# Performance work log

Hardware: AMD Instinct MI355X
Metric: run time of the kernel (lower is better)

Reference implementation:

```python
import jax, jax.numpy as jnp
import numpy as np

N, E, G = 20000, 50000, 64          # nodes, edges, graphs
IN_DIM, EDGE_DIM, H, OUT_DIM = 32, 16, 64, 6
EPS = 1e-5  # BatchNorm eps


def setup_inputs() -> dict:
    key = jax.random.key(0)
    ks = jax.random.split(key, 24)
    s = 0.05
    inp = {
        "x": jax.random.normal(ks[0], (N, IN_DIM), jnp.float32),
        "edge_attr": jax.random.normal(ks[1], (E, EDGE_DIM), jnp.float32),
        "src": jax.random.randint(ks[2], (E,), 0, N, jnp.int32),
        "dst": jax.random.randint(ks[3], (E,), 0, N, jnp.int32),
        "batch": jnp.sort(jax.random.randint(ks[4], (N,), 0, G, jnp.int32)),
        # node encoder
        "Wx": jax.random.normal(ks[5], (IN_DIM, H), jnp.float32) * s,
        "bx": jnp.zeros((H,), jnp.float32),
        # three edge MLPs: edge_dim -> H*H
        "We": jax.random.normal(ks[6], (3, EDGE_DIM, H * H), jnp.float32) * s,
        "be": jnp.zeros((3, H * H), jnp.float32),
        # NNConv root weights / biases
        "Wroot": jax.random.normal(ks[7], (3, H, H), jnp.float32) * s,
        "broot": jnp.zeros((3, H), jnp.float32),
        # BatchNorm (eval mode: running stats)
        "gamma": jnp.ones((3, H), jnp.float32),
        "beta": jnp.zeros((3, H), jnp.float32),
        "run_mean": jnp.zeros((3, H), jnp.float32),
        "run_var": jnp.ones((3, H), jnp.float32),
        # head
        "W1": jax.random.normal(ks[8], (H, H), jnp.float32) * s,
        "b1": jnp.zeros((H,), jnp.float32),
        "W2": jax.random.normal(ks[9], (H, OUT_DIM), jnp.float32) * s,
        "b2": jnp.zeros((OUT_DIM,), jnp.float32),
    }
    return inp


def _segment_mean(vals, idx, num_segments):
    tot = jax.ops.segment_sum(vals, idx, num_segments=num_segments)
    cnt = jax.ops.segment_sum(jnp.ones((vals.shape[0],), vals.dtype), idx,
                              num_segments=num_segments)
    return tot / jnp.maximum(cnt, 1.0)[:, None]


def reference(x, edge_attr, src, dst, batch, Wx, bx, We, be, Wroot, broot,
              gamma, beta, run_mean, run_var, W1, b1, W2, b2):
    h = x @ Wx + bx                                      # (N, H)
    for l in range(3):
        # per-edge H x H weight matrices from the edge MLP
        ew = jax.nn.relu(edge_attr @ We[l] + be[l]).reshape(-1, H, H)  # (E, H, H)
        msg = jnp.einsum('eh,eho->eo', h[src], ew)       # gather + per-edge matvec
        agg = _segment_mean(msg, dst, N)                 # scatter-mean at destinations
        out = agg + h @ Wroot[l] + broot[l]              # NNConv root + bias
        out = jax.nn.relu(out)
        # BatchNorm1d in eval mode (running stats); dropout is identity in eval
        out = gamma[l] * (out - run_mean[l]) * jax.lax.rsqrt(run_var[l] + EPS) + beta[l]
        h = out + h                                      # residual (shapes always match)
    pooled = _segment_mean(h, batch, G)                  # global_mean_pool -> (G, H)
    z = jax.nn.relu(pooled @ W1 + b1)
    return z @ W2 + b2                                   # (G, OUT_DIM)
```

## Files before the change

### kernel.cpp

```cpp
#include <hip/hip_runtime.h>
#include <hip/hip_bf16.h>

typedef _Float16 f16x2 __attribute__((ext_vector_type(2)));
typedef _Float16 f16x8 __attribute__((ext_vector_type(8)));
typedef float    f32x4 __attribute__((ext_vector_type(4)));

#define IN_DIM   32
#define EDGE_DIM 16
#define HDIM     64
#define OUT_DIM  6
#define BN_EPS   1e-5f

__global__ void k_zero(uint4* __restrict__ p, int n16) {
    int i = blockIdx.x * 256 + threadIdx.x;
    if (i < n16) p[i] = make_uint4(0u, 0u, 0u, 0u);
}

__global__ __launch_bounds__(256) void k_setup(
    const float* __restrict__ We, uint4* __restrict__ WeB,
    const float* __restrict__ x, const float* __restrict__ Wx,
    const float* __restrict__ bx, float* __restrict__ h,
    const float* __restrict__ ea, _Float16* __restrict__ eaH,
    const int* __restrict__ dstI, int* __restrict__ degI,
    const int* __restrict__ batch, int* __restrict__ start,
    int N, int E, int G, int PACKB, int ENCB, int PREPB)
{
    __shared__ float w[2048];
    int bid = blockIdx.x;
    int t = threadIdx.x;

    if (bid < PACKB) {
        int layer = bid / 32, chunk = bid % 32;
        int colbase = chunk * 128;
        #pragma unroll
        for (int i = 0; i < 8; ++i) {
            int idx = i * 256 + t;
            int k = idx >> 7, c = idx & 127;
            w[idx] = We[(size_t)layer * 65536 + k * 4096 + colbase + c];
        }
        __syncthreads();
        int tile = t >> 5, lane = t & 31;
        int kslot = lane >> 4, col = tile * 16 + (lane & 15);
        f16x8 v;
        #pragma unroll
        for (int j = 0; j < 8; ++j) v[j] = (_Float16)w[(kslot * 8 + j) * 128 + col];
        WeB[(size_t)layer * 8192 + (size_t)(chunk * 8 + tile) * 32 + lane] = __builtin_bit_cast(uint4, v);
        return;
    }
    bid -= PACKB;
    if (bid < ENCB) {
        int tid = bid * 256 + t;
        int n = tid >> 4, jq = tid & 15;
        if (n >= N) return;
        const float4* W4 = (const float4*)Wx;
        float4 acc = ((const float4*)bx)[jq];
        const float4* xv = (const float4*)(x + (size_t)n * IN_DIM);
        #pragma unroll
        for (int k4 = 0; k4 < 8; ++k4) {
            float4 xk = xv[k4];
            #pragma unroll
            for (int i = 0; i < 4; ++i) {
                float xs = (i == 0) ? xk.x : (i == 1) ? xk.y : (i == 2) ? xk.z : xk.w;
                float4 ww = W4[(k4 * 4 + i) * 16 + jq];
                acc.x += xs * ww.x; acc.y += xs * ww.y; acc.z += xs * ww.z; acc.w += xs * ww.w;
            }
        }
        ((float4*)h)[tid] = acc;
        return;
    }
    bid -= ENCB;
    if (bid < PREPB) {
        int tid = bid * 256 + t;
        int E8 = E * 8;
        if (tid < E8) {
            float2 v = ((const float2*)ea)[tid];
            f16x2 r; r[0] = (_Float16)v.x; r[1] = (_Float16)v.y;
            ((f16x2*)eaH)[tid] = r;
        }
        if (tid < E) atomicAdd(&degI[dstI[tid]], 1);
        return;
    }
    if (t <= G) {
        int lo = 0, hi = N;
        while (lo < hi) { int mid = (lo + hi) >> 1; if (batch[mid] < t) lo = mid + 1; else hi = mid; }
        start[t] = lo;
    }
}

__global__ void k_scan_local(const int* __restrict__ degI, int* __restrict__ rowptr,
                             int* __restrict__ partials, int N) {
    __shared__ int buf[256];
    int b = blockIdx.x, t = threadIdx.x;
    int i = b * 256 + t;
    int v = (i < N) ? degI[i] : 0;
    buf[t] = v;
    __syncthreads();
    #pragma unroll
    for (int ofs = 1; ofs < 256; ofs <<= 1) {
        int xv = (t >= ofs) ? buf[t - ofs] : 0;
        __syncthreads();
        buf[t] += xv;
        __syncthreads();
    }
    if (i < N) rowptr[i] = buf[t] - v;
    if (t == 255) partials[b] = buf[255];
}

__global__ void k_scan_top(int* __restrict__ partials, int nb) {
    __shared__ int buf[256];
    int t = threadIdx.x;
    int v = (t < nb) ? partials[t] : 0;
    buf[t] = v;
    __syncthreads();
    #pragma unroll
    for (int ofs = 1; ofs < 256; ofs <<= 1) {
        int xv = (t >= ofs) ? buf[t - ofs] : 0;
        __syncthreads();
        buf[t] += xv;
        __syncthreads();
    }
    if (t < nb) partials[t] = buf[t] - v;
    if (t == 0) partials[nb] = buf[255];
}

__global__ void k_scan_add(int* __restrict__ rowptr, int* __restrict__ cursor,
                           const int* __restrict__ partials, int N, int nb) {
    int i = blockIdx.x * 256 + threadIdx.x;
    if (i < N) {
        int r = rowptr[i] + partials[blockIdx.x];
        rowptr[i] = r;
        cursor[i] = r;
    }
    if (i == 0) rowptr[N] = partials[nb];
}

__global__ void k_place(const int* __restrict__ dstI, int* __restrict__ cursor,
                        int* __restrict__ eidx, int E) {
    int e = blockIdx.x * 256 + threadIdx.x;
    if (e < E) {
        int p = atomicAdd(&cursor[dstI[e]], 1);
        eidx[p] = e;
    }
}

__global__ __launch_bounds__(256, 6) void k_edge(
    const uint4* __restrict__ eaH,
    const uint4* __restrict__ WeB,
    const float* __restrict__ be,
    const float* __restrict__ hin,
    const int* __restrict__ srcI,
    float* __restrict__ msgP,
    int E)
{
    __shared__ float hsT[32][68];
    __shared__ float beL[2048];
    const int t = threadIdx.x;
    const int l = t & 63;
    const int w = t >> 6;
    const int eg = blockIdx.x >> 1;
    const int hhalf = blockIdx.x & 1;
    const int eb = eg * 64;
    const int hbase = hhalf * 32;

    {
        int egc = min(eb + l, E - 1);
        int s = srcI[egc];
        const float4* hp = (const float4*)(hin + (size_t)s * HDIM + hbase + w * 8);
        float4 a = hp[0], b = hp[1];
        hsT[w*8+0][l] = a.x; hsT[w*8+1][l] = a.y; hsT[w*8+2][l] = a.z; hsT[w*8+3][l] = a.w;
        hsT[w*8+4][l] = b.x; hsT[w*8+5][l] = b.y; hsT[w*8+6][l] = b.z; hsT[w*8+7][l] = b.w;
    }
    {
        const float4* bg = (const float4*)(be + hbase * 64);
        float4* bs = (float4*)beL;
        bs[t] = bg[t];
        bs[256 + t] = bg[256 + t];
    }
    __syncthreads();

    const int gp  = w >> 1;
    const int oh  = w & 1;
    const int ebw = eb + gp * 32;
    const int elw = gp * 32;
    const int g   = l >> 4;
    const int g4  = g * 4;
    const int c16 = l & 15;
    const int obase = oh * 32;

    f16x8 A0 = {}, A1 = {};
    if (g < 2) {
        int e0 = min(ebw + c16, E - 1);
        int e1 = min(ebw + 16 + c16, E - 1);
        A0 = __builtin_bit_cast(f16x8, eaH[(size_t)e0 * 2 + g]);
        A1 = __builtin_bit_cast(f16x8, eaH[(size_t)e1 * 2 + g]);
    }

    f32x4 acc00 = (f32x4)0.f, acc01 = (f32x4)0.f;
    f32x4 acc10 = (f32x4)0.f, acc11 = (f32x4)0.f;

    const uint4* Bbase = WeB + (size_t)(l & 31);
    uint4 Bv0 = Bbase[(size_t)(hbase * 4 + oh * 2 + 0) * 32];
    uint4 Bv1 = Bbase[(size_t)(hbase * 4 + oh * 2 + 1) * 32];

    for (int hh = 0; hh < 32; ++hh) {
        uint4 Bn0, Bn1;
        if (hh < 31) {
            const uint4* Bp = Bbase + (size_t)((hbase + hh + 1) * 4 + oh * 2) * 32;
            Bn0 = Bp[0]; Bn1 = Bp[32];
        }
        float4 p0 = *(const float4*)&hsT[hh][elw + g4];
        float4 p1 = *(const float4*)&hsT[hh][elw + 16 + g4];
        float bia0 = beL[hh * 64 + obase + c16];
        float bia1 = beL[hh * 64 + obase + 16 + c16];
        {
            f16x8 B = __builtin_bit_cast(f16x8, Bv0);
            f32x4 cin = {bia0, bia0, bia0, bia0};
            f32x4 z0 = __builtin_amdgcn_mfma_f32_16x16x32_f16(A0, B, cin, 0, 0, 0);
            f32x4 z1 = __builtin_amdgcn_mfma_f32_16x16x32_f16(A1, B, cin, 0, 0, 0);
            acc00[0] += fmaxf(z0[0], 0.f) * p0.x;
            acc00[1] += fmaxf(z0[1], 0.f) * p0.y;
            acc00[2] += fmaxf(z0[2], 0.f) * p0.z;
            acc00[3] += fmaxf(z0[3], 0.f) * p0.w;
            acc10[0] += fmaxf(z1[0], 0.f) * p1.x;
            acc10[1] += fmaxf(z1[1], 0.f) * p1.y;
            acc10[2] += fmaxf(z1[2], 0.f) * p1.z;
            acc10[3] += fmaxf(z1[3], 0.f) * p1.w;
        }
        {
            f16x8 B = __builtin_bit_cast(f16x8, Bv1);
            f32x4 cin = {bia1, bia1, bia1, bia1};
            f32x4 z0 = __builtin_amdgcn_mfma_f32_16x16x32_f16(A0, B, cin, 0, 0, 0);
            f32x4 z1 = __builtin_amdgcn_mfma_f32_16x16x32_f16(A1, B, cin, 0, 0, 0);
            acc01[0] += fmaxf(z0[0], 0.f) * p0.x;
            acc01[1] += fmaxf(z0[1], 0.f) * p0.y;
            acc01[2] += fmaxf(z0[2], 0.f) * p0.z;
            acc01[3] += fmaxf(z0[3], 0.f) * p0.w;
            acc11[0] += fmaxf(z1[0], 0.f) * p1.x;
            acc11[1] += fmaxf(z1[1], 0.f) * p1.y;
            acc11[2] += fmaxf(z1[2], 0.f) * p1.z;
            acc11[3] += fmaxf(z1[3], 0.f) * p1.w;
        }
        Bv0 = Bn0; Bv1 = Bn1;
    }

    float* mw = msgP + (size_t)hhalf * E * 64;
    #pragma unroll
    for (int grp = 0; grp < 2; ++grp) {
        #pragma unroll
        for (int r = 0; r < 4; ++r) {
            int e = ebw + grp * 16 + g4 + r;
            if (e < E) {
                float v0 = grp == 0 ? acc00[r] : acc10[r];
                float v1 = grp == 0 ? acc01[r] : acc11[r];
                mw[(size_t)e * 64 + obase + c16]      = v0;
                mw[(size_t)e * 64 + obase + 16 + c16] = v1;
            }
        }
    }
}

__global__ void k_update(
    const float* __restrict__ msgP, const int* __restrict__ rowptr,
    const int* __restrict__ eidx,
    const float* __restrict__ hin, const float* __restrict__ Wroot,
    const float* __restrict__ broot, const float* __restrict__ gam,
    const float* __restrict__ bet, const float* __restrict__ rmean,
    const float* __restrict__ rvar, float* __restrict__ hout, int N, int E)
{
    int tid = blockIdx.x * 256 + threadIdx.x;
    int n = tid >> 4, jq = tid & 15;
    if (n >= N) return;
    int r0 = rowptr[n], r1 = rowptr[n + 1];
    float4 s = make_float4(0.f, 0.f, 0.f, 0.f);
    const float4* m4 = (const float4*)msgP;
    for (int i = r0; i < r1; ++i) {
        int eid = eidx[i];
        float4 a = m4[(size_t)eid * 16 + jq];
        float4 b = m4[((size_t)E + eid) * 16 + jq];
        s.x += a.x + b.x; s.y += a.y + b.y; s.z += a.z + b.z; s.w += a.w + b.w;
    }
    float dinv = 1.0f / fmaxf((float)(r1 - r0), 1.0f);
    float4 acc = ((const float4*)broot)[jq];
    acc.x += s.x * dinv; acc.y += s.y * dinv; acc.z += s.z * dinv; acc.w += s.w * dinv;
    const float4* W4 = (const float4*)Wroot;
    const float4* hv = (const float4*)(hin + (size_t)n * HDIM);
    #pragma unroll
    for (int k4 = 0; k4 < 16; ++k4) {
        float4 hk = hv[k4];
        #pragma unroll
        for (int i = 0; i < 4; ++i) {
            float hsc = (i == 0) ? hk.x : (i == 1) ? hk.y : (i == 2) ? hk.z : hk.w;
            float4 ww = W4[(k4 * 4 + i) * 16 + jq];
            acc.x += hsc * ww.x; acc.y += hsc * ww.y; acc.z += hsc * ww.z; acc.w += hsc * ww.w;
        }
    }
    acc.x = fmaxf(acc.x, 0.f); acc.y = fmaxf(acc.y, 0.f);
    acc.z = fmaxf(acc.z, 0.f); acc.w = fmaxf(acc.w, 0.f);
    float4 g4 = ((const float4*)gam)[jq];
    float4 b4 = ((const float4*)bet)[jq];
    float4 mm4 = ((const float4*)rmean)[jq];
    float4 v4 = ((const float4*)rvar)[jq];
    float4 hres = ((const float4*)hin)[tid];
    float4 y;
    y.x = g4.x * (acc.x - mm4.x) * rsqrtf(v4.x + BN_EPS) + b4.x + hres.x;
    y.y = g4.y * (acc.y - mm4.y) * rsqrtf(v4.y + BN_EPS) + b4.y + hres.y;
    y.z = g4.z * (acc.z - mm4.z) * rsqrtf(v4.z + BN_EPS) + b4.z + hres.z;
    y.w = g4.w * (acc.w - mm4.w) * rsqrtf(v4.w + BN_EPS) + b4.w + hres.w;
    ((float4*)hout)[tid] = y;
}

__global__ __launch_bounds__(256) void k_pool_head(
    const float* __restrict__ h, const int* __restrict__ start,
    const float* __restrict__ W1, const float* __restrict__ b1,
    const float* __restrict__ W2, const float* __restrict__ b2,
    float* __restrict__ out)
{
    __shared__ float sums[16][68];
    __shared__ float pl[HDIM];
    __shared__ float zl[HDIM];
    int g = blockIdx.x;
    int s0 = start[g], s1 = start[g + 1];
    int t = threadIdx.x, jq = t & 15, rp = t >> 4;
    float4 acc = make_float4(0.f, 0.f, 0.f, 0.f);
    for (int n = s0 + rp; n < s1; n += 16) {
        float4 v = ((const float4*)h)[(size_t)n * 16 + jq];
        acc.x += v.x; acc.y += v.y; acc.z += v.z; acc.w += v.w;
    }
    *(float4*)&sums[rp][jq * 4] = acc;
    __syncthreads();
    if (t < HDIM) {
        float a = 0.f;
        #pragma unroll
        for (int r = 0; r < 16; ++r) a += sums[r][t];
        float cnt = (float)(s1 - s0);
        pl[t] = a / fmaxf(cnt, 1.0f);
    }
    __syncthreads();
    if (t < HDIM) {
        float a = b1[t];
        #pragma unroll
        for (int k = 0; k < HDIM; ++k) a += pl[k] * W1[k * HDIM + t];
        zl[t] = fmaxf(a, 0.f);
    }
    __syncthreads();
    if (t < OUT_DIM) {
        float a = b2[t];
        #pragma unroll
        for (int k = 0; k < HDIM; ++k) a += zl[k] * W2[k * OUT_DIM + t];
        out[(size_t)g * OUT_DIM + t] = a;
    }
}

extern "C" void kernel_launch(void* const* d_in, const int* in_sizes, int n_in,
                              void* d_out, int out_size, void* d_ws, size_t ws_size,
                              hipStream_t stream) {
    const float* x     = (const float*)d_in[0];
    const float* eattr = (const float*)d_in[1];
    const int*   src   = (const int*)d_in[2];
    const int*   dst   = (const int*)d_in[3];
    const int*   batch = (const int*)d_in[4];
    const float* Wx    = (const float*)d_in[5];
    const float* bx    = (const float*)d_in[6];
    const float* We    = (const float*)d_in[7];
    const float* be    = (const float*)d_in[8];
    const float* Wroot = (const float*)d_in[9];
    const float* broot = (const float*)d_in[10];
    const float* gam   = (const float*)d_in[11];
    const float* bet   = (const float*)d_in[12];
    const float* rmean = (const float*)d_in[13];
    const float* rvar  = (const float*)d_in[14];
    const float* W1    = (const float*)d_in[15];
    const float* b1    = (const float*)d_in[16];
    const float* W2    = (const float*)d_in[17];
    const float* b2    = (const float*)d_in[18];
    float* out = (float*)d_out;

    const int N = in_sizes[0] / IN_DIM;
    const int E = in_sizes[2];
    const int G = out_size / OUT_DIM;

    char* ws = (char*)d_ws;
    size_t off = 0;
    auto alloc = [&](size_t bytes) -> void* {
        void* p = ws + off;
        off = (off + bytes + 255) & ~(size_t)255;
        return p;
    };
    float*    h0      = (float*)alloc((size_t)N * HDIM * 4);
    float*    h1      = (float*)alloc((size_t)N * HDIM * 4);
    _Float16* eaH     = (_Float16*)alloc((size_t)E * 16 * 2);
    uint4*    WeB     = (uint4*)alloc((size_t)3 * 8192 * 16);
    int*      start   = (int*)alloc((size_t)(G + 1) * 4);
    int*      rowptr  = (int*)alloc((size_t)(N + 1) * 4);
    int*      cursor  = (int*)alloc((size_t)N * 4);
    int*      eidx    = (int*)alloc((size_t)E * 4);
    float*    msgP    = (float*)alloc((size_t)2 * E * HDIM * 4);
    int*      degI    = (int*)alloc((size_t)((N + 3) & ~3) * 4);
    const int nb      = (N + 255) / 256;
    int*      partials= (int*)alloc((size_t)(nb + 1) * 4);
    (void)ws_size; (void)n_in;

    const int n16 = ((N + 3) & ~3) / 4;
    k_zero<<<(n16 + 255) / 256, 256, 0, stream>>>((uint4*)degI, n16);

    const int PACKB = 96;
    const int ENCB  = (N * 16 + 255) / 256;
    const int PREPB = (E * 8 + 255) / 256;
    k_setup<<<PACKB + ENCB + PREPB + 1, 256, 0, stream>>>(
        We, WeB, x, Wx, bx, h0, eattr, eaH, dst, degI, batch, start,
        N, E, G, PACKB, ENCB, PREPB);
    k_scan_local<<<nb, 256, 0, stream>>>(degI, rowptr, partials, N);
    k_scan_top<<<1, 256, 0, stream>>>(partials, nb);
    k_scan_add<<<nb, 256, 0, stream>>>(rowptr, cursor, partials, N, nb);
    k_place<<<(E + 255) / 256, 256, 0, stream>>>(dst, cursor, eidx, E);

    const float* hin = h0;
    float* hout = h1;
    const int edgeBlocks = ((E + 63) / 64) * 2;
    for (int l = 0; l < 3; ++l) {
        k_edge<<<edgeBlocks, 256, 0, stream>>>(
            (const uint4*)eaH, WeB + (size_t)l * 8192, be + (size_t)l * 4096,
            hin, src, msgP, E);
        k_update<<<(N * 16 + 255) / 256, 256, 0, stream>>>(
            msgP, rowptr, eidx, hin, Wroot + (size_t)l * 4096, broot + (size_t)l * 64,
            gam + (size_t)l * 64, bet + (size_t)l * 64, rmean + (size_t)l * 64,
            rvar + (size_t)l * 64, hout, N, E);
        float* tmp = hout; hout = (float*)hin; hin = tmp;
    }
    k_pool_head<<<G, 256, 0, stream>>>(hin, start, W1, b1, W2, b2, out);
}
```

Measured before the change: 192.5 us.

## Switch edge kernel to 32x32x16 MFMA and store messages as fp16

The per-edge kernel now issues one 32x32x16 f16 MFMA per hidden index instead of four 16x16x32 MFMAs, whose K-padding left half the lanes' A operands zero. The weight-packing kernel is rewritten to produce the matching operand layout directly from global memory, without a shared-memory transpose. Partial messages are written and read as fp16 instead of fp32, halving the intermediate memory traffic between the edge and update kernels. This lowers message precision before aggregation, and the 16-float accumulator raises register pressure.

```diff
diff --git a/kernel.cpp b/kernel.cpp
--- a/kernel.cpp
+++ b/kernel.cpp
@@ -2,8 +2,10 @@
 #include <hip/hip_bf16.h>
 
 typedef _Float16 f16x2 __attribute__((ext_vector_type(2)));
+typedef _Float16 f16x4 __attribute__((ext_vector_type(4)));
 typedef _Float16 f16x8 __attribute__((ext_vector_type(8)));
 typedef float    f32x4 __attribute__((ext_vector_type(4)));
+typedef float    f32x16 __attribute__((ext_vector_type(16)));
 
 #define IN_DIM   32
 #define EDGE_DIM 16
@@ -25,26 +27,22 @@
     const int* __restrict__ batch, int* __restrict__ start,
     int N, int E, int G, int PACKB, int ENCB, int PREPB)
 {
-    __shared__ float w[2048];
     int bid = blockIdx.x;
     int t = threadIdx.x;
 
     if (bid < PACKB) {
-        int layer = bid / 32, chunk = bid % 32;
-        int colbase = chunk * 128;
-        #pragma unroll
-        for (int i = 0; i < 8; ++i) {
-            int idx = i * 256 + t;
-            int k = idx >> 7, c = idx & 127;
-            w[idx] = We[(size_t)layer * 65536 + k * 4096 + colbase + c];
-        }
-        __syncthreads();
-        int tile = t >> 5, lane = t & 31;
-        int kslot = lane >> 4, col = tile * 16 + (lane & 15);
+        int tid = bid * 256 + t;
+        int tile = tid >> 6, lane = tid & 63;
+        int layer = tile >> 7;
+        int r = tile & 127;
+        int hh = r >> 1, oh = r & 1;
+        int col = hh * 64 + oh * 32 + (lane & 31);
+        int kbase = 8 * (lane >> 5);
+        const float* base = We + (size_t)layer * 65536 + col;
         f16x8 v;
         #pragma unroll
-        for (int j = 0; j < 8; ++j) v[j] = (_Float16)w[(kslot * 8 + j) * 128 + col];
-        WeB[(size_t)layer * 8192 + (size_t)(chunk * 8 + tile) * 32 + lane] = __builtin_bit_cast(uint4, v);
+        for (int j = 0; j < 8; ++j) v[j] = (_Float16)base[(size_t)(kbase + j) * 4096];
+        WeB[(size_t)tile * 64 + lane] = __builtin_bit_cast(uint4, v);
         return;
     }
     bid -= PACKB;
@@ -144,12 +142,12 @@
 }
 
 __global__ __launch_bounds__(256, 6) void k_edge(
-    const uint4* __restrict__ eaH,
+    const uint4* __restrict__ eaH4,
     const uint4* __restrict__ WeB,
     const float* __restrict__ be,
     const float* __restrict__ hin,
     const int* __restrict__ srcI,
-    float* __restrict__ msgP,
+    _Float16* __restrict__ msgP,
     int E)
 {
     __shared__ float hsT[32][68];
@@ -182,85 +180,62 @@
     const int oh  = w & 1;
     const int ebw = eb + gp * 32;
     const int elw = gp * 32;
-    const int g   = l >> 4;
-    const int g4  = g * 4;
-    const int c16 = l & 15;
+    const int row = l & 31;
+    const int kg  = l >> 5;
     const int obase = oh * 32;
 
-    f16x8 A0 = {}, A1 = {};
-    if (g < 2) {
-        int e0 = min(ebw + c16, E - 1);
-        int e1 = min(ebw + 16 + c16, E - 1);
-        A0 = __builtin_bit_cast(f16x8, eaH[(size_t)e0 * 2 + g]);
-        A1 = __builtin_bit_cast(f16x8, eaH[(size_t)e1 * 2 + g]);
-    }
-
-    f32x4 acc00 = (f32x4)0.f, acc01 = (f32x4)0.f;
-    f32x4 acc10 = (f32x4)0.f, acc11 = (f32x4)0.f;
-
-    const uint4* Bbase = WeB + (size_t)(l & 31);
-    uint4 Bv0 = Bbase[(size_t)(hbase * 4 + oh * 2 + 0) * 32];
-    uint4 Bv1 = Bbase[(size_t)(hbase * 4 + oh * 2 + 1) * 32];
+    int ea_e = min(ebw + row, E - 1);
+    f16x8 A = __builtin_bit_cast(f16x8, eaH4[(size_t)ea_e * 2 + kg]);
+
+    float m[16];
+    #pragma unroll
+    for (int j = 0; j < 16; ++j) m[j] = 0.f;
+
+    const uint4* Bb = WeB + (size_t)(hbase * 2 + oh) * 64 + l;
+    uint4 Bv = Bb[0];
 
     for (int hh = 0; hh < 32; ++hh) {
-        uint4 Bn0, Bn1;
-        if (hh < 31) {
-            const uint4* Bp = Bbase + (size_t)((hbase + hh + 1) * 4 + oh * 2) * 32;
-            Bn0 = Bp[0]; Bn1 = Bp[32];
-        }
-        float4 p0 = *(const float4*)&hsT[hh][elw + g4];
-        float4 p1 = *(const float4*)&hsT[hh][elw + 16 + g4];
-        float bia0 = beL[hh * 64 + obase + c16];
-        float bia1 = beL[hh * 64 + obase + 16 + c16];
-        {
-            f16x8 B = __builtin_bit_cast(f16x8, Bv0);
-            f32x4 cin = {bia0, bia0, bia0, bia0};
-            f32x4 z0 = __builtin_amdgcn_mfma_f32_16x16x32_f16(A0, B, cin, 0, 0, 0);
-            f32x4 z1 = __builtin_amdgcn_mfma_f32_16x16x32_f16(A1, B, cin, 0, 0, 0);
-            acc00[0] += fmaxf(z0[0], 0.f) * p0.x;
-            acc00[1] += fmaxf(z0[1], 0.f) * p0.y;
-            acc00[2] += fmaxf(z0[2], 0.f) * p0.z;
-            acc00[3] += fmaxf(z0[3], 0.f) * p0.w;
-            acc10[0] += fmaxf(z1[0], 0.f) * p1.x;
-            acc10[1] += fmaxf(z1[1], 0.f) * p1.y;
-            acc10[2] += fmaxf(z1[2], 0.f) * p1.z;
-            acc10[3] += fmaxf(z1[3], 0.f) * p1.w;
-        }
-        {
-            f16x8 B = __builtin_bit_cast(f16x8, Bv1);
-            f32x4 cin = {bia1, bia1, bia1, bia1};
-            f32x4 z0 = __builtin_amdgcn_mfma_f32_16x16x32_f16(A0, B, cin, 0, 0, 0);
-            f32x4 z1 = __builtin_amdgcn_mfma_f32_16x16x32_f16(A1, B, cin, 0, 0, 0);
-            acc01[0] += fmaxf(z0[0], 0.f) * p0.x;
-            acc01[1] += fmaxf(z0[1], 0.f) * p0.y;
-            acc01[2] += fmaxf(z0[2], 0.f) * p0.z;
-            acc01[3] += fmaxf(z0[3], 0.f) * p0.w;
-            acc11[0] += fmaxf(z1[0], 0.f) * p1.x;
-            acc11[1] += fmaxf(z1[1], 0.f) * p1.y;
-            acc11[2] += fmaxf(z1[2], 0.f) * p1.z;
-            acc11[3] += fmaxf(z1[3], 0.f) * p1.w;
-        }
-        Bv0 = Bn0; Bv1 = Bn1;
-    }
-
-    float* mw = msgP + (size_t)hhalf * E * 64;
+        uint4 Bn;
+        if (hh < 31) Bn = Bb[(size_t)(hh + 1) * 128];
+        float bias = beL[hh * 64 + obase + (l & 31)];
+        f32x16 cin;
+        #pragma unroll
+        for (int j = 0; j < 16; ++j) cin[j] = bias;
+        f32x16 z = __builtin_amdgcn_mfma_f32_32x32x16_f16(
+            A, __builtin_bit_cast(f16x8, Bv), cin, 0, 0, 0);
+        float4 q0 = *(const float4*)&hsT[hh][elw + 4 * kg + 0];
+        float4 q1 = *(const float4*)&hsT[hh][elw + 4 * kg + 8];
+        float4 q2 = *(const float4*)&hsT[hh][elw + 4 * kg + 16];
+        float4 q3 = *(const float4*)&hsT[hh][elw + 4 * kg + 24];
+        m[0]  += fmaxf(z[0],  0.f) * q0.x;
+        m[1]  += fmaxf(z[1],  0.f) * q0.y;
+        m[2]  += fmaxf(z[2],  0.f) * q0.z;
+        m[3]  += fmaxf(z[3],  0.f) * q0.w;
+        m[4]  += fmaxf(z[4],  0.f) * q1.x;
+        m[5]  += fmaxf(z[5],  0.f) * q1.y;
+        m[6]  += fmaxf(z[6],  0.f) * q1.z;
+        m[7]  += fmaxf(z[7],  0.f) * q1.w;
+        m[8]  += fmaxf(z[8],  0.f) * q2.x;
+        m[9]  += fmaxf(z[9],  0.f) * q2.y;
+        m[10] += fmaxf(z[10], 0.f) * q2.z;
+        m[11] += fmaxf(z[11], 0.f) * q2.w;
+        m[12] += fmaxf(z[12], 0.f) * q3.x;
+        m[13] += fmaxf(z[13], 0.f) * q3.y;
+        m[14] += fmaxf(z[14], 0.f) * q3.z;
+        m[15] += fmaxf(z[15], 0.f) * q3.w;
+        Bv = Bn;
+    }
+
+    _Float16* mw = msgP + (size_t)hhalf * E * 64 + obase + (l & 31);
     #pragma unroll
-    for (int grp = 0; grp < 2; ++grp) {
-        #pragma unroll
-        for (int r = 0; r < 4; ++r) {
-            int e = ebw + grp * 16 + g4 + r;
-            if (e < E) {
-                float v0 = grp == 0 ? acc00[r] : acc10[r];
-                float v1 = grp == 0 ? acc01[r] : acc11[r];
-                mw[(size_t)e * 64 + obase + c16]      = v0;
-                mw[(size_t)e * 64 + obase + 16 + c16] = v1;
-            }
-        }
+    for (int j = 0; j < 16; ++j) {
+        int e = ebw + (j & 3) + 8 * (j >> 2) + 4 * kg;
+        if (e < E) mw[(size_t)e * 64] = (_Float16)m[j];
     }
 }
 
 __global__ void k_update(
-    const float* __restrict__ msgP, const int* __restrict__ rowptr,
+    const _Float16* __restrict__ msgP, const int* __restrict__ rowptr,
     const int* __restrict__ eidx,
     const float* __restrict__ hin, const float* __restrict__ Wroot,
     const float* __restrict__ broot, const float* __restrict__ gam,
@@ -272,12 +247,15 @@
     if (n >= N) return;
     int r0 = rowptr[n], r1 = rowptr[n + 1];
     float4 s = make_float4(0.f, 0.f, 0.f, 0.f);
-    const float4* m4 = (const float4*)msgP;
+    const f16x4* m4 = (const f16x4*)msgP;
     for (int i = r0; i < r1; ++i) {
         int eid = eidx[i];
-        float4 a = m4[(size_t)eid * 16 + jq];
-        float4 b = m4[((size_t)E + eid) * 16 + jq];
-        s.x += a.x + b.x; s.y += a.y + b.y; s.z += a.z + b.z; s.w += a.w + b.w;
+        f16x4 a = m4[(size_t)eid * 16 + jq];
+        f16x4 b = m4[((size_t)E + eid) * 16 + jq];
+        s.x += (float)a[0] + (float)b[0];
+        s.y += (float)a[1] + (float)b[1];
+        s.z += (float)a[2] + (float)b[2];
+        s.w += (float)a[3] + (float)b[3];
     }
     float dinv = 1.0f / fmaxf((float)(r1 - r0), 1.0f);
     float4 acc = ((const float4*)broot)[jq];
@@ -389,12 +367,12 @@
     float*    h0      = (float*)alloc((size_t)N * HDIM * 4);
     float*    h1      = (float*)alloc((size_t)N * HDIM * 4);
     _Float16* eaH     = (_Float16*)alloc((size_t)E * 16 * 2);
-    uint4*    WeB     = (uint4*)alloc((size_t)3 * 8192 * 16);
+    uint4*    WeB     = (uint4*)alloc((size_t)3 * 128 * 64 * 16);
     int*      start   = (int*)alloc((size_t)(G + 1) * 4);
     int*      rowptr  = (int*)alloc((size_t)(N + 1) * 4);
     int*      cursor  = (int*)alloc((size_t)N * 4);
     int*      eidx    = (int*)alloc((size_t)E * 4);
-    float*    msgP    = (float*)alloc((size_t)2 * E * HDIM * 4);
+    _Float16* msgP    = (_Float16*)alloc((size_t)2 * E * HDIM * 2);
     int*      degI    = (int*)alloc((size_t)((N + 3) & ~3) * 4);
     const int nb      = (N + 255) / 256;
     int*      partials= (int*)alloc((size_t)(nb + 1) * 4);
```

After: 195.2 us. No clear change (+1.4%).
